# Kernel tuning notes

Hardware: AMD Instinct MI355X
Metric: run time of the kernel (lower is better)

## Reference

```python
import jax, jax.numpy as jnp
import numpy as np

N_NODES = 100000
N_EDGES = 3200000
IN_DIM = 4
HID = 128
OUT_DIM = 4


def setup_inputs() -> dict:
    key = jax.random.key(0)
    ks = jax.random.split(key, 16)
    x = jax.random.normal(ks[0], (N_NODES, IN_DIM), dtype=jnp.float32)
    edge_index = jax.random.randint(ks[1], (2, N_EDGES), 0, N_NODES, dtype=jnp.int32)
    hidden_mask = jax.random.randint(ks[2], (N_NODES,), 0, 2) > 0
    def glorot(k, shape):
        fan_in, fan_out = shape[0], shape[1]
        s = jnp.sqrt(6.0 / (fan_in + fan_out))
        return jax.random.uniform(k, shape, jnp.float32, -s, s)
    return {
        "x": x,
        "edge_index": edge_index,
        "hidden_mask": hidden_mask,
        "W0": glorot(ks[3], (IN_DIM, HID)), "b0": jnp.zeros((HID,), jnp.float32),
        "res_W": glorot(ks[4], (IN_DIM, HID)), "res_b": jnp.zeros((HID,), jnp.float32),
        "W1": glorot(ks[5], (HID, HID)), "b1": jnp.zeros((HID,), jnp.float32),
        "W2": glorot(ks[6], (HID, HID)), "b2": jnp.zeros((HID,), jnp.float32),
        "fc_W": glorot(ks[7], (HID, OUT_DIM)), "fc_b": jnp.zeros((OUT_DIM,), jnp.float32),
    }


def _gcn_norm(edge_index, num_nodes):
    # add self loops, compute symmetric normalization (PyG GCNConv default)
    loop = jnp.arange(num_nodes, dtype=edge_index.dtype)
    src = jnp.concatenate([edge_index[0], loop])
    dst = jnp.concatenate([edge_index[1], loop])
    deg = jax.ops.segment_sum(jnp.ones_like(dst, dtype=jnp.float32), dst,
                              num_segments=num_nodes)
    dis = jnp.where(deg > 0, jax.lax.rsqrt(deg), 0.0)  # deg^{-1/2}, inf -> 0
    norm = dis[src] * dis[dst]  # [E + N]
    return src, dst, norm


def _gcn_conv(h, W, b, src, dst, norm, num_nodes):
    h = h @ W                       # [N, out]
    msg = h[src] * norm[:, None]    # gather + scale, [E+N, out]
    agg = jax.ops.segment_sum(msg, dst, num_segments=num_nodes)
    return agg + b


def reference(x, edge_index, hidden_mask, W0, b0, res_W, res_b, W1, b1, W2, b2, fc_W, fc_b):
    n = x.shape[0]
    src, dst, norm = _gcn_norm(edge_index, n)
    # mask input features (mask broadcast over 4 feature cols)
    h = jnp.where(hidden_mask[:, None], x, 0.0)
    # layer 0: in_dim != hidden -> linear residual
    out0 = _gcn_conv(h, W0, b0, src, dst, norm, n)
    h = jax.nn.relu(out0 + (h @ res_W + res_b))
    # layers 1,2: identity residual
    h = jax.nn.relu(_gcn_conv(h, W1, b1, src, dst, norm, n) + h)
    h = jax.nn.relu(_gcn_conv(h, W2, b2, src, dst, norm, n) + h)
    x_out = h @ fc_W + fc_b
    return (x_out, hidden_mask)
```

## Files before the change

### kernel.cpp

```cpp
#include <hip/hip_runtime.h>
#include <hip/hip_bf16.h>
#include <stdint.h>

#define HID 128
#define NPART 8
#define NCHUNK 256
#define MCHUNK 4096
#define LBITS 10
#define SBITS 22

__global__ void detect_mask_kernel(const unsigned char* __restrict__ p, int nbytes,
                                   int nfloat, int* __restrict__ flags) {
  int stride = blockDim.x * gridDim.x;
  for (int i = blockIdx.x * blockDim.x + threadIdx.x; i < nbytes; i += stride) {
    if ((i & 3) && p[i] != 0) { atomicOr(&flags[0], 1); break; }
  }
  const float* fp = (const float*)p;
  for (int i = blockIdx.x * blockDim.x + threadIdx.x; i < nfloat; i += stride) {
    float f = fp[i];
    if (!(f == 0.0f || f == 1.0f)) { atomicOr(&flags[1], 1); break; }
  }
}

__global__ void expand_mask_h0(const void* __restrict__ maskp, const float4* __restrict__ x4,
                               const int* __restrict__ flags, const float* __restrict__ dis,
                               float* __restrict__ maskout, float* __restrict__ cvec,
                               float4* __restrict__ h0s, int N) {
  int i = blockIdx.x * blockDim.x + threadIdx.x;
  if (i >= N) return;
  float m;
  if (flags[0] == 0)      m = (((const int*)maskp)[i] != 0) ? 1.f : 0.f;
  else if (flags[1] == 0) m = (((const float*)maskp)[i] != 0.f) ? 1.f : 0.f;
  else                    m = (((const unsigned char*)maskp)[i] != 0) ? 1.f : 0.f;
  maskout[i] = m;
  float4 xv = x4[i];
  float4 h0 = make_float4(m * xv.x, m * xv.y, m * xv.z, m * xv.w);
  float* cv = cvec + (size_t)i * 8;
  cv[4] = h0.x; cv[5] = h0.y; cv[6] = h0.z; cv[7] = h0.w;
  float d = dis[i];
  h0s[i] = make_float4(d * h0.x, d * h0.y, d * h0.z, d * h0.w);
}

__global__ void init_gcur_kernel(int* __restrict__ gcur, int n, int CAPB) {
  int i = blockIdx.x * blockDim.x + threadIdx.x;
  if (i < n) gcur[i] = i * CAPB;
}

__global__ void radixA_kernel(const int* __restrict__ src, const int* __restrict__ dst,
                              int* __restrict__ gcur, uint32_t* __restrict__ bdata,
                              int nbin, int CAPB, int E) {
  __shared__ uint32_t sv[MCHUNK];
  __shared__ uint16_t sb[MCHUNK];
  __shared__ int bcnt[1024], boff[1024], gbase[1024];
  __shared__ int wsum[4];
  int t = threadIdx.x;
  int base = blockIdx.x * MCHUNK;
  int m = E - base; if (m > MCHUNK) m = MCHUNK;
  for (int i = t; i < 1024; i += 256) bcnt[i] = 0;
  __syncthreads();
  uint32_t pk[16]; short bn[16];
#pragma unroll
  for (int j = 0; j < 16; j++) {
    int i = base + t + j * 256;
    if (i < base + m) {
      int d = __builtin_nontemporal_load(&dst[i]);
      int s = __builtin_nontemporal_load(&src[i]);
      int b = d >> LBITS;
      pk[j] = ((uint32_t)(d & ((1 << LBITS) - 1)) << SBITS) | (uint32_t)s;
      bn[j] = (short)b;
      atomicAdd(&bcnt[b], 1);
    } else bn[j] = -1;
  }
  __syncthreads();
  {
    int lane = t & 63, w = t >> 6, i0 = t * 4;
    int v0 = bcnt[i0], v1 = bcnt[i0 + 1], v2 = bcnt[i0 + 2], v3 = bcnt[i0 + 3];
    int ts = v0 + v1 + v2 + v3, sc = ts;
    for (int d = 1; d < 64; d <<= 1) { int x = __shfl_up(sc, d, 64); if (lane >= d) sc += x; }
    if (lane == 63) wsum[w] = sc;
    __syncthreads();
    int wo = 0;
    for (int k = 0; k < w; k++) wo += wsum[k];
    int excl = wo + sc - ts;
    boff[i0] = excl; boff[i0 + 1] = excl + v0;
    boff[i0 + 2] = excl + v0 + v1; boff[i0 + 3] = excl + v0 + v1 + v2;
  }
  __syncthreads();
  for (int i = t; i < nbin; i += 256) {
    int c = bcnt[i];
    gbase[i] = c ? atomicAdd(&gcur[i], c) : 0;
  }
  __syncthreads();
  for (int i = t; i < nbin; i += 256) bcnt[i] = boff[i];
  __syncthreads();
#pragma unroll
  for (int j = 0; j < 16; j++) {
    if (bn[j] >= 0) {
      int p = atomicAdd(&bcnt[bn[j]], 1);
      sv[p] = pk[j];
      sb[p] = (uint16_t)bn[j];
    }
  }
  __syncthreads();
  for (int i = t; i < m; i += 256) {
    int b = sb[i];
    int gp = gbase[b] + (i - boff[b]);
    if (gp < (b + 1) * CAPB) bdata[gp] = sv[i];
  }
}

__global__ void bucket_meta_kernel(const int* __restrict__ gcur, int* __restrict__ bstart,
                                   int nbin, int CAPB) {
  __shared__ int wsum[4];
  int t = threadIdx.x, lane = t & 63, w = t >> 6, i0 = t * 4;
  int v[4];
#pragma unroll
  for (int q = 0; q < 4; q++) {
    int i = i0 + q;
    int c = 0;
    if (i < nbin) {
      c = gcur[i] - i * CAPB;
      if (c > CAPB) c = CAPB;
    }
    v[q] = c;
  }
  int ts = v[0] + v[1] + v[2] + v[3], sc = ts;
  for (int d = 1; d < 64; d <<= 1) { int x = __shfl_up(sc, d, 64); if (lane >= d) sc += x; }
  if (lane == 63) wsum[w] = sc;
  __syncthreads();
  int wo = 0;
  for (int k = 0; k < w; k++) wo += wsum[k];
  int excl = wo + sc - ts;
  int e[4] = {excl, excl + v[0], excl + v[0] + v[1], excl + v[0] + v[1] + v[2]};
#pragma unroll
  for (int q = 0; q < 4; q++)
    if (i0 + q < nbin) bstart[i0 + q] = e[q];
  if (t == 255) bstart[nbin] = wo + sc;
}

__global__ void radixB_kernel(const uint32_t* __restrict__ bdata, const int* __restrict__ gcur,
                              const int* __restrict__ bstart, int CAPB,
                              int* __restrict__ off, float* __restrict__ dis,
                              int* __restrict__ csr, int N, int E) {
  __shared__ int cnt[1024], loff[1024];
  __shared__ int wsum[4];
  int b = blockIdx.x, t = threadIdx.x;
  int cb = gcur[b] - b * CAPB; if (cb > CAPB) cb = CAPB;
  int gb = bstart[b];
  const uint32_t* bd = bdata + (size_t)b * CAPB;
  for (int i = t; i < 1024; i += 256) cnt[i] = 0;
  __syncthreads();
  for (int i = t; i < cb; i += 256) atomicAdd(&cnt[bd[i] >> SBITS], 1);
  __syncthreads();
  {
    int lane = t & 63, w = t >> 6, i0 = t * 4;
    int v0 = cnt[i0], v1 = cnt[i0 + 1], v2 = cnt[i0 + 2], v3 = cnt[i0 + 3];
    int ts = v0 + v1 + v2 + v3, sc = ts;
    for (int d = 1; d < 64; d <<= 1) { int x = __shfl_up(sc, d, 64); if (lane >= d) sc += x; }
    if (lane == 63) wsum[w] = sc;
    __syncthreads();
    int wo = 0;
    for (int k = 0; k < w; k++) wo += wsum[k];
    int e0 = wo + sc - ts;
    int e1 = e0 + v0, e2 = e1 + v1, e3 = e2 + v2;
    loff[i0] = e0; loff[i0 + 1] = e1; loff[i0 + 2] = e2; loff[i0 + 3] = e3;
    int d0 = b * 1024 + i0;
    if (d0 + 0 < N) { off[d0 + 0] = gb + e0; dis[d0 + 0] = rsqrtf((float)v0 + 1.0f); }
    if (d0 + 1 < N) { off[d0 + 1] = gb + e1; dis[d0 + 1] = rsqrtf((float)v1 + 1.0f); }
    if (d0 + 2 < N) { off[d0 + 2] = gb + e2; dis[d0 + 2] = rsqrtf((float)v2 + 1.0f); }
    if (d0 + 3 < N) { off[d0 + 3] = gb + e3; dis[d0 + 3] = rsqrtf((float)v3 + 1.0f); }
  }
  if (b == 0 && t == 0) off[N] = E;
  __syncthreads();
  for (int i = t; i < 1024; i += 256) cnt[i] = loff[i];
  __syncthreads();
  for (int i = t; i < cb; i += 256) {
    uint32_t v = bd[i];
    int p = atomicAdd(&cnt[v >> SBITS], 1);
    csr[gb + p] = (int)(v & ((1u << SBITS) - 1));
  }
}

__global__ void scan1_kernel(const int* __restrict__ cnt, int* __restrict__ off,
                             int* __restrict__ bsum, float* __restrict__ dis, int N) {
  __shared__ int wsum[4];
  int t = threadIdx.x, lane = t & 63, w = t >> 6;
  int base = blockIdx.x * 1024 + t * 4;
  int v0 = (base + 0 < N) ? cnt[base + 0] : 0;
  int v1 = (base + 1 < N) ? cnt[base + 1] : 0;
  int v2 = (base + 2 < N) ? cnt[base + 2] : 0;
  int v3 = (base + 3 < N) ? cnt[base + 3] : 0;
  if (dis) {
    if (base + 0 < N) dis[base + 0] = rsqrtf((float)v0 + 1.0f);
    if (base + 1 < N) dis[base + 1] = rsqrtf((float)v1 + 1.0f);
    if (base + 2 < N) dis[base + 2] = rsqrtf((float)v2 + 1.0f);
    if (base + 3 < N) dis[base + 3] = rsqrtf((float)v3 + 1.0f);
  }
  int ts = v0 + v1 + v2 + v3;
  int sc = ts;
  for (int d = 1; d < 64; d <<= 1) {
    int x = __shfl_up(sc, d, 64);
    if (lane >= d) sc += x;
  }
  if (lane == 63) wsum[w] = sc;
  __syncthreads();
  int wo = 0;
  for (int i = 0; i < w; i++) wo += wsum[i];
  int excl = wo + sc - ts;
  if (base + 0 < N) off[base + 0] = excl;
  if (base + 1 < N) off[base + 1] = excl + v0;
  if (base + 2 < N) off[base + 2] = excl + v0 + v1;
  if (base + 3 < N) off[base + 3] = excl + v0 + v1 + v2;
  if (t == 255) bsum[blockIdx.x] = wo + sc;
}

__global__ void scan2_kernel(int* __restrict__ bsum, int nb) {
  if (threadIdx.x == 0 && blockIdx.x == 0) {
    int run = 0;
    for (int i = 0; i < nb; i++) { int v = bsum[i]; bsum[i] = run; run += v; }
  }
}

__global__ void scan3_kernel(int* __restrict__ off, const int* __restrict__ bsum,
                             int* __restrict__ cur, int N, int E) {
  int i = blockIdx.x * blockDim.x + threadIdx.x;
  if (i < N) {
    int o = off[i] + bsum[i >> 10];
    off[i] = o;
    if (cur) cur[i] = o;
  }
  if (i == 0) off[N] = E;
}

__global__ void hist_part_kernel(const int* __restrict__ dst, int* __restrict__ cnt,
                                 int E, int N) {
  int p = blockIdx.x & (NPART - 1);
  int chunk = blockIdx.x >> 3;
  int lo = (int)((long long)p * N / NPART);
  int hi = (int)((long long)(p + 1) * N / NPART);
  int stride = NCHUNK * 256;
  for (int e = chunk * 256 + threadIdx.x; e < E; e += stride) {
    int d = __builtin_nontemporal_load(&dst[e]);
    if (d >= lo && d < hi) atomicAdd(&cnt[d], 1);
  }
}

__global__ void fill_part_kernel(const int* __restrict__ src, const int* __restrict__ dst,
                                 int* __restrict__ cur, int* __restrict__ csr, int E, int N) {
  int p = blockIdx.x & (NPART - 1);
  int chunk = blockIdx.x >> 3;
  int lo = (int)((long long)p * N / NPART);
  int hi = (int)((long long)(p + 1) * N / NPART);
  int stride = NCHUNK * 256;
  for (int e = chunk * 256 + threadIdx.x; e < E; e += stride) {
    int d = __builtin_nontemporal_load(&dst[e]);
    if (d >= lo && d < hi) {
      int s = __builtin_nontemporal_load(&src[e]);
      int pos = atomicAdd(&cur[d], 1);
      csr[pos] = s;
    }
  }
}

__global__ void l0_agg_kernel(const float4* __restrict__ h0s, const float* __restrict__ dis,
                              const int* __restrict__ off, const int* __restrict__ csr,
                              float* __restrict__ cvec, int N) {
  int n = blockIdx.x * blockDim.x + threadIdx.x;
  if (n >= N) return;
  float4 a = h0s[n];
  int e0 = off[n], e1 = off[n + 1];
  int i = e0;
  for (; i < e1 && (i & 3); i++) {
    float4 v = h0s[csr[i]];
    a.x += v.x; a.y += v.y; a.z += v.z; a.w += v.w;
  }
  for (; i + 4 <= e1; i += 4) {
    int4 c = *(const int4*)&csr[i];
    float4 v0 = h0s[c.x], v1 = h0s[c.y], v2 = h0s[c.z], v3 = h0s[c.w];
    a.x += v0.x + v1.x + v2.x + v3.x;
    a.y += v0.y + v1.y + v2.y + v3.y;
    a.z += v0.z + v1.z + v2.z + v3.z;
    a.w += v0.w + v1.w + v2.w + v3.w;
  }
  for (; i < e1; i++) {
    float4 v = h0s[csr[i]];
    a.x += v.x; a.y += v.y; a.z += v.z; a.w += v.w;
  }
  float dn = dis[n];
  float* cv = cvec + (size_t)n * 8;
  cv[0] = dn * a.x; cv[1] = dn * a.y; cv[2] = dn * a.z; cv[3] = dn * a.w;
}

__global__ void l0_combine_kernel(const float* __restrict__ cvec, const float* __restrict__ W0,
                                  const float* __restrict__ b0, const float* __restrict__ resW,
                                  const float* __restrict__ resb, const float* __restrict__ dis,
                                  float* __restrict__ h1, __hip_bfloat16* __restrict__ hbout) {
  int idx = blockIdx.x * blockDim.x + threadIdx.x;
  int n = idx >> 7, c = idx & 127;
  const float* cv = cvec + (size_t)n * 8;
  float acc = b0[c] + resb[c];
#pragma unroll
  for (int k = 0; k < 4; k++) {
    acc += cv[k] * W0[k * HID + c];
    acc += cv[4 + k] * resW[k * HID + c];
  }
  float v = fmaxf(acc, 0.0f);
  h1[idx] = v;
  if (hbout) hbout[idx] = __float2bfloat16(dis[n] * v);
}

#define ACC1(W) { a0 += __uint_as_float((W) << 16); a1 += __uint_as_float((W) & 0xffff0000u); }

__device__ __forceinline__ void gather_tile(const uint32_t* __restrict__ hb,
                                            const float* __restrict__ dis,
                                            const int* __restrict__ off,
                                            const int* __restrict__ csr,
                                            float* __restrict__ ash, int n0, int N) {
  int t = threadIdx.x, lane = t & 63, wv = t >> 6;
  for (int ln = wv * 16; ln < wv * 16 + 16; ln++) {
    int node = n0 + ln;
    float a0 = 0.f, a1 = 0.f;
    if (node < N) {
      uint32_t w = hb[(size_t)node * 64 + lane];
      a0 = __uint_as_float(w << 16);
      a1 = __uint_as_float(w & 0xffff0000u);
      int e0 = off[node], e1 = off[node + 1];
      int i = e0;
      for (; i < e1 && (i & 3); i++) {
        uint32_t ww = hb[(size_t)csr[i] * 64 + lane];
        ACC1(ww)
      }
      for (; i + 16 <= e1; i += 16) {
        int4 c0 = *(const int4*)&csr[i];
        int4 c1 = *(const int4*)&csr[i + 4];
        int4 c2 = *(const int4*)&csr[i + 8];
        int4 c3 = *(const int4*)&csr[i + 12];
        uint32_t w0 = hb[(size_t)c0.x * 64 + lane];
        uint32_t w1 = hb[(size_t)c0.y * 64 + lane];
        uint32_t w2 = hb[(size_t)c0.z * 64 + lane];
        uint32_t w3 = hb[(size_t)c0.w * 64 + lane];
        uint32_t w4 = hb[(size_t)c1.x * 64 + lane];
        uint32_t w5 = hb[(size_t)c1.y * 64 + lane];
        uint32_t w6 = hb[(size_t)c1.z * 64 + lane];
        uint32_t w7 = hb[(size_t)c1.w * 64 + lane];
        uint32_t w8 = hb[(size_t)c2.x * 64 + lane];
        uint32_t w9 = hb[(size_t)c2.y * 64 + lane];
        uint32_t wa = hb[(size_t)c2.z * 64 + lane];
        uint32_t wb = hb[(size_t)c2.w * 64 + lane];
        uint32_t wc = hb[(size_t)c3.x * 64 + lane];
        uint32_t wd = hb[(size_t)c3.y * 64 + lane];
        uint32_t we = hb[(size_t)c3.z * 64 + lane];
        uint32_t wf = hb[(size_t)c3.w * 64 + lane];
        ACC1(w0) ACC1(w1) ACC1(w2) ACC1(w3) ACC1(w4) ACC1(w5) ACC1(w6) ACC1(w7)
        ACC1(w8) ACC1(w9) ACC1(wa) ACC1(wb) ACC1(wc) ACC1(wd) ACC1(we) ACC1(wf)
      }
      for (; i + 4 <= e1; i += 4) {
        int4 c = *(const int4*)&csr[i];
        uint32_t w0 = hb[(size_t)c.x * 64 + lane];
        uint32_t w1 = hb[(size_t)c.y * 64 + lane];
        uint32_t w2 = hb[(size_t)c.z * 64 + lane];
        uint32_t w3 = hb[(size_t)c.w * 64 + lane];
        ACC1(w0) ACC1(w1) ACC1(w2) ACC1(w3)
      }
      for (; i < e1; i++) {
        uint32_t ww = hb[(size_t)csr[i] * 64 + lane];
        ACC1(ww)
      }
      float dn = dis[node];
      a0 *= dn; a1 *= dn;
    }
    *(float2*)&ash[ln * HID + 2 * lane] = make_float2(a0, a1);
  }
}

__global__ void agg_gemm_kernel(const uint32_t* __restrict__ hb, const float* __restrict__ dis,
                                const int* __restrict__ off, const int* __restrict__ csr,
                                const float* __restrict__ hres,
                                const float* __restrict__ W, const float* __restrict__ b,
                                float* __restrict__ hout, __hip_bfloat16* __restrict__ hbout,
                                int N) {
  __shared__ float ash[64 * HID];
  int t = threadIdx.x;
  int n0 = blockIdx.x * 64;
  gather_tile(hb, dis, off, csr, ash, n0, N);
  __syncthreads();
  int tc = t & 31;
  int tn = t >> 5;
  float acc[8][4];
#pragma unroll
  for (int j = 0; j < 8; j++)
#pragma unroll
    for (int q = 0; q < 4; q++) acc[j][q] = 0.0f;

  for (int k = 0; k < HID; k += 4) {
    float4 w0 = *(const float4*)&W[(k + 0) * HID + tc * 4];
    float4 w1 = *(const float4*)&W[(k + 1) * HID + tc * 4];
    float4 w2 = *(const float4*)&W[(k + 2) * HID + tc * 4];
    float4 w3 = *(const float4*)&W[(k + 3) * HID + tc * 4];
#pragma unroll
    for (int j = 0; j < 8; j++) {
      float4 a = *(const float4*)&ash[(tn * 8 + j) * HID + k];
      acc[j][0] += a.x * w0.x + a.y * w1.x + a.z * w2.x + a.w * w3.x;
      acc[j][1] += a.x * w0.y + a.y * w1.y + a.z * w2.y + a.w * w3.y;
      acc[j][2] += a.x * w0.z + a.y * w1.z + a.z * w2.z + a.w * w3.z;
      acc[j][3] += a.x * w0.w + a.y * w1.w + a.z * w2.w + a.w * w3.w;
    }
  }
  float4 bv = *(const float4*)&b[tc * 4];
#pragma unroll
  for (int j = 0; j < 8; j++) {
    int gn = n0 + tn * 8 + j;
    if (gn < N) {
      float4 hv = *(const float4*)&hres[(size_t)gn * HID + tc * 4];
      float4 o;
      o.x = fmaxf(acc[j][0] + bv.x + hv.x, 0.0f);
      o.y = fmaxf(acc[j][1] + bv.y + hv.y, 0.0f);
      o.z = fmaxf(acc[j][2] + bv.z + hv.z, 0.0f);
      o.w = fmaxf(acc[j][3] + bv.w + hv.w, 0.0f);
      *(float4*)&hout[(size_t)gn * HID + tc * 4] = o;
      float dnn = dis[gn];
      __hip_bfloat162 p01 = __float22bfloat162_rn(make_float2(dnn * o.x, dnn * o.y));
      __hip_bfloat162 p23 = __float22bfloat162_rn(make_float2(dnn * o.z, dnn * o.w));
      *(__hip_bfloat162*)&hbout[(size_t)gn * HID + tc * 4] = p01;
      *(__hip_bfloat162*)&hbout[(size_t)gn * HID + tc * 4 + 2] = p23;
    }
  }
}

__global__ void agg_gemm_fc_kernel(const uint32_t* __restrict__ hb, const float* __restrict__ dis,
                                   const int* __restrict__ off, const int* __restrict__ csr,
                                   const float* __restrict__ hres,
                                   const float* __restrict__ W, const float* __restrict__ b,
                                   const float* __restrict__ fcW, const float* __restrict__ fcb,
                                   float* __restrict__ out, int N) {
  __shared__ float ash[64 * HID];
  int t = threadIdx.x;
  int n0 = blockIdx.x * 64;
  gather_tile(hb, dis, off, csr, ash, n0, N);
  __syncthreads();
  int tc = t & 31;
  int tn = t >> 5;
  float acc[8][4];
#pragma unroll
  for (int j = 0; j < 8; j++)
#pragma unroll
    for (int q = 0; q < 4; q++) acc[j][q] = 0.0f;

  for (int k = 0; k < HID; k += 4) {
    float4 w0 = *(const float4*)&W[(k + 0) * HID + tc * 4];
    float4 w1 = *(const float4*)&W[(k + 1) * HID + tc * 4];
    float4 w2 = *(const float4*)&W[(k + 2) * HID + tc * 4];
    float4 w3 = *(const float4*)&W[(k + 3) * HID + tc * 4];
#pragma unroll
    for (int j = 0; j < 8; j++) {
      float4 a = *(const float4*)&ash[(tn * 8 + j) * HID + k];
      acc[j][0] += a.x * w0.x + a.y * w1.x + a.z * w2.x + a.w * w3.x;
      acc[j][1] += a.x * w0.y + a.y * w1.y + a.z * w2.y + a.w * w3.y;
      acc[j][2] += a.x * w0.z + a.y * w1.z + a.z * w2.z + a.w * w3.z;
      acc[j][3] += a.x * w0.w + a.y * w1.w + a.z * w2.w + a.w * w3.w;
    }
  }
  float4 f0 = *(const float4*)&fcW[(tc * 4 + 0) * 4];
  float4 f1 = *(const float4*)&fcW[(tc * 4 + 1) * 4];
  float4 f2 = *(const float4*)&fcW[(tc * 4 + 2) * 4];
  float4 f3 = *(const float4*)&fcW[(tc * 4 + 3) * 4];
  float4 bv = *(const float4*)&b[tc * 4];
  float4 fb = *(const float4*)&fcb[0];
#pragma unroll
  for (int j = 0; j < 8; j++) {
    int gn = n0 + tn * 8 + j;
    float4 o = make_float4(0.f, 0.f, 0.f, 0.f);
    if (gn < N) {
      float4 hv = *(const float4*)&hres[(size_t)gn * HID + tc * 4];
      o.x = fmaxf(acc[j][0] + bv.x + hv.x, 0.0f);
      o.y = fmaxf(acc[j][1] + bv.y + hv.y, 0.0f);
      o.z = fmaxf(acc[j][2] + bv.z + hv.z, 0.0f);
      o.w = fmaxf(acc[j][3] + bv.w + hv.w, 0.0f);
    }
    float r0 = o.x * f0.x + o.y * f1.x + o.z * f2.x + o.w * f3.x;
    float r1 = o.x * f0.y + o.y * f1.y + o.z * f2.y + o.w * f3.y;
    float r2 = o.x * f0.z + o.y * f1.z + o.z * f2.z + o.w * f3.z;
    float r3 = o.x * f0.w + o.y * f1.w + o.z * f2.w + o.w * f3.w;
#pragma unroll
    for (int d = 1; d < 32; d <<= 1) {
      r0 += __shfl_xor(r0, d, 64);
      r1 += __shfl_xor(r1, d, 64);
      r2 += __shfl_xor(r2, d, 64);
      r3 += __shfl_xor(r3, d, 64);
    }
    if (tc == 0 && gn < N)
      *(float4*)&out[(size_t)gn * 4] =
          make_float4(r0 + fb.x, r1 + fb.y, r2 + fb.z, r3 + fb.w);
  }
}

__global__ void agg_hid_kernel(const float* __restrict__ h, const float* __restrict__ dis,
                               const int* __restrict__ off, const int* __restrict__ csr,
                               float* __restrict__ out, int N) {
  int node = blockIdx.x * 4 + (threadIdx.x >> 6);
  int lane = threadIdx.x & 63;
  if (node >= N) return;
  float dn = dis[node];
  const float* hrow = h + (size_t)node * HID;
  float a0 = dn * hrow[lane];
  float a1 = dn * hrow[lane + 64];
  int e0 = off[node], e1 = off[node + 1];
  for (int i = e0; i < e1; i++) {
    int s = csr[i];
    float d = dis[s];
    const float* hs = h + (size_t)s * HID;
    a0 += d * hs[lane];
    a1 += d * hs[lane + 64];
  }
  out[(size_t)node * HID + lane] = dn * a0;
  out[(size_t)node * HID + lane + 64] = dn * a1;
}

__global__ void gemm_resid_relu_kernel(const float* __restrict__ ag, float* __restrict__ hout,
                                       const float* __restrict__ hres,
                                       const float* __restrict__ W, const float* __restrict__ b,
                                       int N) {
  __shared__ float ash[64 * HID];
  int t = threadIdx.x;
  int n0 = blockIdx.x * 64;
  for (int i = t; i < 64 * HID; i += 256) {
    int gn = n0 + (i >> 7);
    ash[i] = (gn < N) ? ag[(size_t)gn * HID + (i & 127)] : 0.0f;
  }
  __syncthreads();
  int tc = t & 31;
  int tn = t >> 5;
  float acc[8][4];
#pragma unroll
  for (int j = 0; j < 8; j++)
#pragma unroll
    for (int q = 0; q < 4; q++) acc[j][q] = 0.0f;
  for (int k = 0; k < HID; k += 4) {
    float4 w0 = *(const float4*)&W[(k + 0) * HID + tc * 4];
    float4 w1 = *(const float4*)&W[(k + 1) * HID + tc * 4];
    float4 w2 = *(const float4*)&W[(k + 2) * HID + tc * 4];
    float4 w3 = *(const float4*)&W[(k + 3) * HID + tc * 4];
#pragma unroll
    for (int j = 0; j < 8; j++) {
      float4 a = *(const float4*)&ash[(tn * 8 + j) * HID + k];
      acc[j][0] += a.x * w0.x + a.y * w1.x + a.z * w2.x + a.w * w3.x;
      acc[j][1] += a.x * w0.y + a.y * w1.y + a.z * w2.y + a.w * w3.y;
      acc[j][2] += a.x * w0.z + a.y * w1.z + a.z * w2.z + a.w * w3.z;
      acc[j][3] += a.x * w0.w + a.y * w1.w + a.z * w2.w + a.w * w3.w;
    }
  }
  float4 bv = *(const float4*)&b[tc * 4];
#pragma unroll
  for (int j = 0; j < 8; j++) {
    int gn = n0 + tn * 8 + j;
    if (gn < N) {
      float4 hv = *(const float4*)&hres[(size_t)gn * HID + tc * 4];
      float4 o;
      o.x = fmaxf(acc[j][0] + bv.x + hv.x, 0.0f);
      o.y = fmaxf(acc[j][1] + bv.y + hv.y, 0.0f);
      o.z = fmaxf(acc[j][2] + bv.z + hv.z, 0.0f);
      o.w = fmaxf(acc[j][3] + bv.w + hv.w, 0.0f);
      *(float4*)&hout[(size_t)gn * HID + tc * 4] = o;
    }
  }
}

__global__ void gemm_resid_fc_kernel(const float* __restrict__ ag,
                                     const float* __restrict__ hres,
                                     const float* __restrict__ W, const float* __restrict__ b,
                                     const float* __restrict__ fcW, const float* __restrict__ fcb,
                                     float* __restrict__ out, int N) {
  __shared__ float ash[64 * HID];
  int t = threadIdx.x;
  int n0 = blockIdx.x * 64;
  for (int i = t; i < 64 * HID; i += 256) {
    int gn = n0 + (i >> 7);
    ash[i] = (gn < N) ? ag[(size_t)gn * HID + (i & 127)] : 0.0f;
  }
  __syncthreads();
  int tc = t & 31;
  int tn = t >> 5;
  float acc[8][4];
#pragma unroll
  for (int j = 0; j < 8; j++)
#pragma unroll
    for (int q = 0; q < 4; q++) acc[j][q] = 0.0f;
  for (int k = 0; k < HID; k += 4) {
    float4 w0 = *(const float4*)&W[(k + 0) * HID + tc * 4];
    float4 w1 = *(const float4*)&W[(k + 1) * HID + tc * 4];
    float4 w2 = *(const float4*)&W[(k + 2) * HID + tc * 4];
    float4 w3 = *(const float4*)&W[(k + 3) * HID + tc * 4];
#pragma unroll
    for (int j = 0; j < 8; j++) {
      float4 a = *(const float4*)&ash[(tn * 8 + j) * HID + k];
      acc[j][0] += a.x * w0.x + a.y * w1.x + a.z * w2.x + a.w * w3.x;
      acc[j][1] += a.x * w0.y + a.y * w1.y + a.z * w2.y + a.w * w3.y;
      acc[j][2] += a.x * w0.z + a.y * w1.z + a.z * w2.z + a.w * w3.z;
      acc[j][3] += a.x * w0.w + a.y * w1.w + a.z * w2.w + a.w * w3.w;
    }
  }
  float4 f0 = *(const float4*)&fcW[(tc * 4 + 0) * 4];
  float4 f1 = *(const float4*)&fcW[(tc * 4 + 1) * 4];
  float4 f2 = *(const float4*)&fcW[(tc * 4 + 2) * 4];
  float4 f3 = *(const float4*)&fcW[(tc * 4 + 3) * 4];
  float4 bv = *(const float4*)&b[tc * 4];
  float4 fb = *(const float4*)&fcb[0];
#pragma unroll
  for (int j = 0; j < 8; j++) {
    int gn = n0 + tn * 8 + j;
    float4 o = make_float4(0.f, 0.f, 0.f, 0.f);
    if (gn < N) {
      float4 hv = *(const float4*)&hres[(size_t)gn * HID + tc * 4];
      o.x = fmaxf(acc[j][0] + bv.x + hv.x, 0.0f);
      o.y = fmaxf(acc[j][1] + bv.y + hv.y, 0.0f);
      o.z = fmaxf(acc[j][2] + bv.z + hv.z, 0.0f);
      o.w = fmaxf(acc[j][3] + bv.w + hv.w, 0.0f);
    }
    float r0 = o.x * f0.x + o.y * f1.x + o.z * f2.x + o.w * f3.x;
    float r1 = o.x * f0.y + o.y * f1.y + o.z * f2.y + o.w * f3.y;
    float r2 = o.x * f0.z + o.y * f1.z + o.z * f2.z + o.w * f3.z;
    float r3 = o.x * f0.w + o.y * f1.w + o.z * f2.w + o.w * f3.w;
#pragma unroll
    for (int d = 1; d < 32; d <<= 1) {
      r0 += __shfl_xor(r0, d, 64);
      r1 += __shfl_xor(r1, d, 64);
      r2 += __shfl_xor(r2, d, 64);
      r3 += __shfl_xor(r3, d, 64);
    }
    if (tc == 0 && gn < N)
      *(float4*)&out[(size_t)gn * 4] =
          make_float4(r0 + fb.x, r1 + fb.y, r2 + fb.z, r3 + fb.w);
  }
}

extern "C" void kernel_launch(void* const* d_in, const int* in_sizes, int n_in,
                              void* d_out, int out_size, void* d_ws, size_t ws_size,
                              hipStream_t stream) {
  const float* x = (const float*)d_in[0];
  const int* edge = (const int*)d_in[1];
  const void* maskp = d_in[2];
  const float* W0 = (const float*)d_in[3];
  const float* b0 = (const float*)d_in[4];
  const float* resW = (const float*)d_in[5];
  const float* resb = (const float*)d_in[6];
  const float* W1 = (const float*)d_in[7];
  const float* b1 = (const float*)d_in[8];
  const float* W2 = (const float*)d_in[9];
  const float* b2 = (const float*)d_in[10];
  const float* fcW = (const float*)d_in[11];
  const float* fcb = (const float*)d_in[12];
  float* out = (float*)d_out;

  int N = in_sizes[0] / 4;
  int E = in_sizes[1] / 2;
  const int* srcp = edge;
  const int* dstp = edge + E;

  char* ws = (char*)d_ws;
  size_t cursor = 0;
  auto alloc = [&](size_t bytes) { char* p = ws + cursor; cursor += (bytes + 511) & ~(size_t)511; return p; };
  int* flags = (int*)alloc(16);
  int* cnt = (int*)alloc((size_t)N * 4);
  float* dis = (float*)alloc((size_t)N * 4);
  int* off = (int*)alloc((size_t)(N + 1) * 4);
  int* bsum = (int*)alloc(1024);
  int nbin = (N + 1023) >> 10;
  int* gcur = (int*)alloc((size_t)(nbin + 1) * 4);
  int* bstart = (int*)alloc((size_t)(nbin + 1) * 4);
  int* csr = (int*)alloc((size_t)E * 4);
  float* h0s = (float*)alloc((size_t)N * 4 * 4);
  float* cvec = (float*)alloc((size_t)N * 8 * 4);
  float* buf0 = (float*)alloc((size_t)N * HID * 4);
  float* buf1 = (float*)alloc((size_t)N * HID * 4);
  size_t base_cursor = cursor;
  __hip_bfloat16* hb1 = (__hip_bfloat16*)alloc((size_t)N * HID * 2);
  __hip_bfloat16* hb2 = (__hip_bfloat16*)alloc((size_t)N * HID * 2);
  bool use_bf16 = (cursor <= ws_size);
  if (!use_bf16) {
    hb1 = nullptr; hb2 = nullptr;
    if (base_cursor > ws_size) return;
  }

  long long expect = (long long)E / (nbin > 0 ? nbin : 1);
  int CAPB = (int)((((expect * 5) / 4 + 127) / 64) * 64);
  if (CAPB < 256) CAPB = 256;
  size_t bdata_bytes = (size_t)nbin * CAPB * 4;
  bool use_radix = (N <= (1 << SBITS)) && (nbin <= 1024) &&
                   (bdata_bytes <= (size_t)N * HID * 4);
  uint32_t* bdata = (uint32_t*)buf1;

  int nThreadsN = (N + 255) / 256;
  int ngemm = (N + 63) / 64;

  hipMemsetAsync(flags, 0, 16, stream);
  detect_mask_kernel<<<256, 256, 0, stream>>>((const unsigned char*)maskp, N, N / 4, flags);

  if (use_radix) {
    init_gcur_kernel<<<(nbin + 255) / 256, 256, 0, stream>>>(gcur, nbin, CAPB);
    radixA_kernel<<<(E + MCHUNK - 1) / MCHUNK, 256, 0, stream>>>(srcp, dstp, gcur, bdata,
                                                                 nbin, CAPB, E);
    bucket_meta_kernel<<<1, 256, 0, stream>>>(gcur, bstart, nbin, CAPB);
    radixB_kernel<<<nbin, 256, 0, stream>>>(bdata, gcur, bstart, CAPB, off, dis, csr, N, E);
  } else {
    hipMemsetAsync(cnt, 0, (size_t)N * 4, stream);
    int nb = (N + 1023) / 1024;
    hist_part_kernel<<<NPART * NCHUNK, 256, 0, stream>>>(dstp, cnt, E, N);
    scan1_kernel<<<nb, 256, 0, stream>>>(cnt, off, bsum, dis, N);
    scan2_kernel<<<1, 64, 0, stream>>>(bsum, nb);
    scan3_kernel<<<nThreadsN, 256, 0, stream>>>(off, bsum, cnt, N, E);
    fill_part_kernel<<<NPART * NCHUNK, 256, 0, stream>>>(srcp, dstp, cnt, csr, E, N);
  }

  expand_mask_h0<<<nThreadsN, 256, 0, stream>>>(maskp, (const float4*)x, flags, dis,
                                                out + (size_t)N * 4, cvec, (float4*)h0s, N);

  l0_agg_kernel<<<nThreadsN, 256, 0, stream>>>((const float4*)h0s, dis, off, csr, cvec, N);
  l0_combine_kernel<<<(N * HID + 255) / 256, 256, 0, stream>>>(cvec, W0, b0, resW, resb, dis,
                                                               buf0, hb1);

  if (use_bf16) {
    agg_gemm_kernel<<<ngemm, 256, 0, stream>>>((const uint32_t*)hb1, dis, off, csr,
                                               buf0, W1, b1, buf1, hb2, N);
    agg_gemm_fc_kernel<<<ngemm, 256, 0, stream>>>((const uint32_t*)hb2, dis, off, csr,
                                                  buf1, W2, b2, fcW, fcb, out, N);
  } else {
    agg_hid_kernel<<<(N + 3) / 4, 256, 0, stream>>>(buf0, dis, off, csr, buf1, N);
    gemm_resid_relu_kernel<<<ngemm, 256, 0, stream>>>(buf1, buf1, buf0, W1, b1, N);
    agg_hid_kernel<<<(N + 3) / 4, 256, 0, stream>>>(buf1, dis, off, csr, buf0, N);
    gemm_resid_fc_kernel<<<ngemm, 256, 0, stream>>>(buf0, buf1, W2, b2, fcW, fcb, out, N);
  }
}
```

Before: 612.6 us.

## Sort CSR neighbors by source chunk and split fused aggregate-GEMM kernels

The radix CSR build now uses 512-node destination bins and sub-sorts each node's neighbor list by coarse source chunk (8 chunks), so gathers walk memory in a more ordered way and hit cache better. The fused gather+GEMM kernels are split into a standalone bf16 aggregation kernel (one wave per node) followed by a GEMM kernel. The fp32 residual copy is dropped: the residual is rebuilt from the dis-scaled bf16 features times a new sqrt(deg) array (rdis). This adds extra kernel launches and an fp32 intermediate round trip, and the residual loses precision to bf16.

```diff
diff --git a/kernel.cpp b/kernel.cpp
--- a/kernel.cpp
+++ b/kernel.cpp
@@ -6,8 +6,9 @@
 #define NPART 8
 #define NCHUNK 256
 #define MCHUNK 4096
-#define LBITS 10
+#define LBITS 9
 #define SBITS 22
+#define NCH 8
 
 __global__ void detect_mask_kernel(const unsigned char* __restrict__ p, int nbytes,
                                    int nfloat, int* __restrict__ flags) {
@@ -141,43 +142,65 @@
 __global__ void radixB_kernel(const uint32_t* __restrict__ bdata, const int* __restrict__ gcur,
                               const int* __restrict__ bstart, int CAPB,
                               int* __restrict__ off, float* __restrict__ dis,
-                              int* __restrict__ csr, int N, int E) {
-  __shared__ int cnt[1024], loff[1024];
+                              float* __restrict__ rdis, int* __restrict__ csr,
+                              int N, int E, int cshift) {
+  __shared__ int cnt[4096], loff[4096];
   __shared__ int wsum[4];
   int b = blockIdx.x, t = threadIdx.x;
   int cb = gcur[b] - b * CAPB; if (cb > CAPB) cb = CAPB;
   int gb = bstart[b];
   const uint32_t* bd = bdata + (size_t)b * CAPB;
-  for (int i = t; i < 1024; i += 256) cnt[i] = 0;
-  __syncthreads();
-  for (int i = t; i < cb; i += 256) atomicAdd(&cnt[bd[i] >> SBITS], 1);
-  __syncthreads();
-  {
-    int lane = t & 63, w = t >> 6, i0 = t * 4;
-    int v0 = cnt[i0], v1 = cnt[i0 + 1], v2 = cnt[i0 + 2], v3 = cnt[i0 + 3];
-    int ts = v0 + v1 + v2 + v3, sc = ts;
-    for (int d = 1; d < 64; d <<= 1) { int x = __shfl_up(sc, d, 64); if (lane >= d) sc += x; }
-    if (lane == 63) wsum[w] = sc;
-    __syncthreads();
-    int wo = 0;
-    for (int k = 0; k < w; k++) wo += wsum[k];
-    int e0 = wo + sc - ts;
-    int e1 = e0 + v0, e2 = e1 + v1, e3 = e2 + v2;
-    loff[i0] = e0; loff[i0 + 1] = e1; loff[i0 + 2] = e2; loff[i0 + 3] = e3;
-    int d0 = b * 1024 + i0;
-    if (d0 + 0 < N) { off[d0 + 0] = gb + e0; dis[d0 + 0] = rsqrtf((float)v0 + 1.0f); }
-    if (d0 + 1 < N) { off[d0 + 1] = gb + e1; dis[d0 + 1] = rsqrtf((float)v1 + 1.0f); }
-    if (d0 + 2 < N) { off[d0 + 2] = gb + e2; dis[d0 + 2] = rsqrtf((float)v2 + 1.0f); }
-    if (d0 + 3 < N) { off[d0 + 3] = gb + e3; dis[d0 + 3] = rsqrtf((float)v3 + 1.0f); }
-  }
-  if (b == 0 && t == 0) off[N] = E;
-  __syncthreads();
-  for (int i = t; i < 1024; i += 256) cnt[i] = loff[i];
-  __syncthreads();
+  for (int i = t; i < 4096; i += 256) cnt[i] = 0;
+  __syncthreads();
+  const uint32_t smask = (1u << SBITS) - 1;
   for (int i = t; i < cb; i += 256) {
     uint32_t v = bd[i];
-    int p = atomicAdd(&cnt[v >> SBITS], 1);
-    csr[gb + p] = (int)(v & ((1u << SBITS) - 1));
+    int ld = v >> SBITS;
+    int src = (int)(v & smask);
+    atomicAdd(&cnt[(ld << 3) | (src >> cshift)], 1);
+  }
+  __syncthreads();
+  int lane = t & 63, w = t >> 6;
+  int loc[16];
+  int s = 0;
+  int base16 = t * 16;
+#pragma unroll
+  for (int q = 0; q < 16; q++) { loc[q] = cnt[base16 + q]; s += loc[q]; }
+  int sc = s;
+  for (int d = 1; d < 64; d <<= 1) { int x = __shfl_up(sc, d, 64); if (lane >= d) sc += x; }
+  if (lane == 63) wsum[w] = sc;
+  __syncthreads();
+  int wo = 0;
+  for (int k = 0; k < w; k++) wo += wsum[k];
+  int excl = wo + sc - s;
+  {
+    int run = excl;
+#pragma unroll
+    for (int q = 0; q < 16; q++) { loff[base16 + q] = run; run += loc[q]; }
+  }
+  int c0 = loc[0] + loc[1] + loc[2] + loc[3] + loc[4] + loc[5] + loc[6] + loc[7];
+  int c1 = loc[8] + loc[9] + loc[10] + loc[11] + loc[12] + loc[13] + loc[14] + loc[15];
+  int dst0 = b * (1 << LBITS) + 2 * t;
+  if (dst0 < N) {
+    off[dst0] = gb + excl;
+    dis[dst0] = rsqrtf((float)c0 + 1.0f);
+    rdis[dst0] = sqrtf((float)c0 + 1.0f);
+  }
+  if (dst0 + 1 < N) {
+    off[dst0 + 1] = gb + excl + c0;
+    dis[dst0 + 1] = rsqrtf((float)c1 + 1.0f);
+    rdis[dst0 + 1] = sqrtf((float)c1 + 1.0f);
+  }
+  if (b == 0 && t == 0) off[N] = E;
+  __syncthreads();
+  for (int i = t; i < 4096; i += 256) cnt[i] = loff[i];
+  __syncthreads();
+  for (int i = t; i < cb; i += 256) {
+    uint32_t v = bd[i];
+    int ld = v >> SBITS;
+    int src = (int)(v & smask);
+    int p = atomicAdd(&cnt[(ld << 3) | (src >> cshift)], 1);
+    csr[gb + p] = src;
   }
 }
 
@@ -305,193 +328,53 @@
     acc += cv[4 + k] * resW[k * HID + c];
   }
   float v = fmaxf(acc, 0.0f);
-  h1[idx] = v;
+  if (h1) h1[idx] = v;
   if (hbout) hbout[idx] = __float2bfloat16(dis[n] * v);
 }
 
 #define ACC1(W) { a0 += __uint_as_float((W) << 16); a1 += __uint_as_float((W) & 0xffff0000u); }
-
-__device__ __forceinline__ void gather_tile(const uint32_t* __restrict__ hb,
-                                            const float* __restrict__ dis,
-                                            const int* __restrict__ off,
-                                            const int* __restrict__ csr,
-                                            float* __restrict__ ash, int n0, int N) {
-  int t = threadIdx.x, lane = t & 63, wv = t >> 6;
-  for (int ln = wv * 16; ln < wv * 16 + 16; ln++) {
-    int node = n0 + ln;
-    float a0 = 0.f, a1 = 0.f;
-    if (node < N) {
-      uint32_t w = hb[(size_t)node * 64 + lane];
-      a0 = __uint_as_float(w << 16);
-      a1 = __uint_as_float(w & 0xffff0000u);
-      int e0 = off[node], e1 = off[node + 1];
-      int i = e0;
-      for (; i < e1 && (i & 3); i++) {
-        uint32_t ww = hb[(size_t)csr[i] * 64 + lane];
-        ACC1(ww)
-      }
-      for (; i + 16 <= e1; i += 16) {
-        int4 c0 = *(const int4*)&csr[i];
-        int4 c1 = *(const int4*)&csr[i + 4];
-        int4 c2 = *(const int4*)&csr[i + 8];
-        int4 c3 = *(const int4*)&csr[i + 12];
-        uint32_t w0 = hb[(size_t)c0.x * 64 + lane];
-        uint32_t w1 = hb[(size_t)c0.y * 64 + lane];
-        uint32_t w2 = hb[(size_t)c0.z * 64 + lane];
-        uint32_t w3 = hb[(size_t)c0.w * 64 + lane];
-        uint32_t w4 = hb[(size_t)c1.x * 64 + lane];
-        uint32_t w5 = hb[(size_t)c1.y * 64 + lane];
-        uint32_t w6 = hb[(size_t)c1.z * 64 + lane];
-        uint32_t w7 = hb[(size_t)c1.w * 64 + lane];
-        uint32_t w8 = hb[(size_t)c2.x * 64 + lane];
-        uint32_t w9 = hb[(size_t)c2.y * 64 + lane];
-        uint32_t wa = hb[(size_t)c2.z * 64 + lane];
-        uint32_t wb = hb[(size_t)c2.w * 64 + lane];
-        uint32_t wc = hb[(size_t)c3.x * 64 + lane];
-        uint32_t wd = hb[(size_t)c3.y * 64 + lane];
-        uint32_t we = hb[(size_t)c3.z * 64 + lane];
-        uint32_t wf = hb[(size_t)c3.w * 64 + lane];
-        ACC1(w0) ACC1(w1) ACC1(w2) ACC1(w3) ACC1(w4) ACC1(w5) ACC1(w6) ACC1(w7)
-        ACC1(w8) ACC1(w9) ACC1(wa) ACC1(wb) ACC1(wc) ACC1(wd) ACC1(we) ACC1(wf)
-      }
-      for (; i + 4 <= e1; i += 4) {
-        int4 c = *(const int4*)&csr[i];
-        uint32_t w0 = hb[(size_t)c.x * 64 + lane];
-        uint32_t w1 = hb[(size_t)c.y * 64 + lane];
-        uint32_t w2 = hb[(size_t)c.z * 64 + lane];
-        uint32_t w3 = hb[(size_t)c.w * 64 + lane];
-        ACC1(w0) ACC1(w1) ACC1(w2) ACC1(w3)
-      }
-      for (; i < e1; i++) {
-        uint32_t ww = hb[(size_t)csr[i] * 64 + lane];
-        ACC1(ww)
-      }
-      float dn = dis[node];
-      a0 *= dn; a1 *= dn;
-    }
-    *(float2*)&ash[ln * HID + 2 * lane] = make_float2(a0, a1);
-  }
-}
-
-__global__ void agg_gemm_kernel(const uint32_t* __restrict__ hb, const float* __restrict__ dis,
-                                const int* __restrict__ off, const int* __restrict__ csr,
-                                const float* __restrict__ hres,
-                                const float* __restrict__ W, const float* __restrict__ b,
-                                float* __restrict__ hout, __hip_bfloat16* __restrict__ hbout,
-                                int N) {
-  __shared__ float ash[64 * HID];
-  int t = threadIdx.x;
-  int n0 = blockIdx.x * 64;
-  gather_tile(hb, dis, off, csr, ash, n0, N);
-  __syncthreads();
-  int tc = t & 31;
-  int tn = t >> 5;
-  float acc[8][4];
-#pragma unroll
-  for (int j = 0; j < 8; j++)
-#pragma unroll
-    for (int q = 0; q < 4; q++) acc[j][q] = 0.0f;
-
-  for (int k = 0; k < HID; k += 4) {
-    float4 w0 = *(const float4*)&W[(k + 0) * HID + tc * 4];
-    float4 w1 = *(const float4*)&W[(k + 1) * HID + tc * 4];
-    float4 w2 = *(const float4*)&W[(k + 2) * HID + tc * 4];
-    float4 w3 = *(const float4*)&W[(k + 3) * HID + tc * 4];
-#pragma unroll
-    for (int j = 0; j < 8; j++) {
-      float4 a = *(const float4*)&ash[(tn * 8 + j) * HID + k];
-      acc[j][0] += a.x * w0.x + a.y * w1.x + a.z * w2.x + a.w * w3.x;
-      acc[j][1] += a.x * w0.y + a.y * w1.y + a.z * w2.y + a.w * w3.y;
-      acc[j][2] += a.x * w0.z + a.y * w1.z + a.z * w2.z + a.w * w3.z;
-      acc[j][3] += a.x * w0.w + a.y * w1.w + a.z * w2.w + a.w * w3.w;
-    }
-  }
-  float4 bv = *(const float4*)&b[tc * 4];
-#pragma unroll
-  for (int j = 0; j < 8; j++) {
-    int gn = n0 + tn * 8 + j;
-    if (gn < N) {
-      float4 hv = *(const float4*)&hres[(size_t)gn * HID + tc * 4];
-      float4 o;
-      o.x = fmaxf(acc[j][0] + bv.x + hv.x, 0.0f);
-      o.y = fmaxf(acc[j][1] + bv.y + hv.y, 0.0f);
-      o.z = fmaxf(acc[j][2] + bv.z + hv.z, 0.0f);
-      o.w = fmaxf(acc[j][3] + bv.w + hv.w, 0.0f);
-      *(float4*)&hout[(size_t)gn * HID + tc * 4] = o;
-      float dnn = dis[gn];
-      __hip_bfloat162 p01 = __float22bfloat162_rn(make_float2(dnn * o.x, dnn * o.y));
-      __hip_bfloat162 p23 = __float22bfloat162_rn(make_float2(dnn * o.z, dnn * o.w));
-      *(__hip_bfloat162*)&hbout[(size_t)gn * HID + tc * 4] = p01;
-      *(__hip_bfloat162*)&hbout[(size_t)gn * HID + tc * 4 + 2] = p23;
-    }
-  }
-}
-
-__global__ void agg_gemm_fc_kernel(const uint32_t* __restrict__ hb, const float* __restrict__ dis,
-                                   const int* __restrict__ off, const int* __restrict__ csr,
-                                   const float* __restrict__ hres,
-                                   const float* __restrict__ W, const float* __restrict__ b,
-                                   const float* __restrict__ fcW, const float* __restrict__ fcb,
-                                   float* __restrict__ out, int N) {
-  __shared__ float ash[64 * HID];
-  int t = threadIdx.x;
-  int n0 = blockIdx.x * 64;
-  gather_tile(hb, dis, off, csr, ash, n0, N);
-  __syncthreads();
-  int tc = t & 31;
-  int tn = t >> 5;
-  float acc[8][4];
-#pragma unroll
-  for (int j = 0; j < 8; j++)
-#pragma unroll
-    for (int q = 0; q < 4; q++) acc[j][q] = 0.0f;
-
-  for (int k = 0; k < HID; k += 4) {
-    float4 w0 = *(const float4*)&W[(k + 0) * HID + tc * 4];
-    float4 w1 = *(const float4*)&W[(k + 1) * HID + tc * 4];
-    float4 w2 = *(const float4*)&W[(k + 2) * HID + tc * 4];
-    float4 w3 = *(const float4*)&W[(k + 3) * HID + tc * 4];
-#pragma unroll
-    for (int j = 0; j < 8; j++) {
-      float4 a = *(const float4*)&ash[(tn * 8 + j) * HID + k];
-      acc[j][0] += a.x * w0.x + a.y * w1.x + a.z * w2.x + a.w * w3.x;
-      acc[j][1] += a.x * w0.y + a.y * w1.y + a.z * w2.y + a.w * w3.y;
-      acc[j][2] += a.x * w0.z + a.y * w1.z + a.z * w2.z + a.w * w3.z;
-      acc[j][3] += a.x * w0.w + a.y * w1.w + a.z * w2.w + a.w * w3.w;
-    }
-  }
-  float4 f0 = *(const float4*)&fcW[(tc * 4 + 0) * 4];
-  float4 f1 = *(const float4*)&fcW[(tc * 4 + 1) * 4];
-  float4 f2 = *(const float4*)&fcW[(tc * 4 + 2) * 4];
-  float4 f3 = *(const float4*)&fcW[(tc * 4 + 3) * 4];
-  float4 bv = *(const float4*)&b[tc * 4];
-  float4 fb = *(const float4*)&fcb[0];
-#pragma unroll
-  for (int j = 0; j < 8; j++) {
-    int gn = n0 + tn * 8 + j;
-    float4 o = make_float4(0.f, 0.f, 0.f, 0.f);
-    if (gn < N) {
-      float4 hv = *(const float4*)&hres[(size_t)gn * HID + tc * 4];
-      o.x = fmaxf(acc[j][0] + bv.x + hv.x, 0.0f);
-      o.y = fmaxf(acc[j][1] + bv.y + hv.y, 0.0f);
-      o.z = fmaxf(acc[j][2] + bv.z + hv.z, 0.0f);
-      o.w = fmaxf(acc[j][3] + bv.w + hv.w, 0.0f);
-    }
-    float r0 = o.x * f0.x + o.y * f1.x + o.z * f2.x + o.w * f3.x;
-    float r1 = o.x * f0.y + o.y * f1.y + o.z * f2.y + o.w * f3.y;
-    float r2 = o.x * f0.z + o.y * f1.z + o.z * f2.z + o.w * f3.z;
-    float r3 = o.x * f0.w + o.y * f1.w + o.z * f2.w + o.w * f3.w;
-#pragma unroll
-    for (int d = 1; d < 32; d <<= 1) {
-      r0 += __shfl_xor(r0, d, 64);
-      r1 += __shfl_xor(r1, d, 64);
-      r2 += __shfl_xor(r2, d, 64);
-      r3 += __shfl_xor(r3, d, 64);
-    }
-    if (tc == 0 && gn < N)
-      *(float4*)&out[(size_t)gn * 4] =
-          make_float4(r0 + fb.x, r1 + fb.y, r2 + fb.z, r3 + fb.w);
-  }
+__global__ void agg_hid_bf16_kernel(const uint32_t* __restrict__ hb, const float* __restrict__ dis,
+                                    const int* __restrict__ off, const int* __restrict__ csr,
+                                    float* __restrict__ out, int N) {
+  int node = blockIdx.x * 4 + (threadIdx.x >> 6);
+  int lane = threadIdx.x & 63;
+  if (node >= N) return;
+  uint32_t w = hb[(size_t)node * 64 + lane];
+  float a0 = __uint_as_float(w << 16);
+  float a1 = __uint_as_float(w & 0xffff0000u);
+  int e0 = off[node], e1 = off[node + 1];
+  int i = e0;
+  for (; i < e1 && (i & 3); i++) {
+    uint32_t ww = hb[(size_t)csr[i] * 64 + lane];
+    ACC1(ww)
+  }
+  for (; i + 8 <= e1; i += 8) {
+    int4 c0 = *(const int4*)&csr[i];
+    int4 c1 = *(const int4*)&csr[i + 4];
+    uint32_t w0 = hb[(size_t)c0.x * 64 + lane];
+    uint32_t w1 = hb[(size_t)c0.y * 64 + lane];
+    uint32_t w2 = hb[(size_t)c0.z * 64 + lane];
+    uint32_t w3 = hb[(size_t)c0.w * 64 + lane];
+    uint32_t w4 = hb[(size_t)c1.x * 64 + lane];
+    uint32_t w5 = hb[(size_t)c1.y * 64 + lane];
+    uint32_t w6 = hb[(size_t)c1.z * 64 + lane];
+    uint32_t w7 = hb[(size_t)c1.w * 64 + lane];
+    ACC1(w0) ACC1(w1) ACC1(w2) ACC1(w3) ACC1(w4) ACC1(w5) ACC1(w6) ACC1(w7)
+  }
+  for (; i + 4 <= e1; i += 4) {
+    int4 c = *(const int4*)&csr[i];
+    uint32_t w0 = hb[(size_t)c.x * 64 + lane];
+    uint32_t w1 = hb[(size_t)c.y * 64 + lane];
+    uint32_t w2 = hb[(size_t)c.z * 64 + lane];
+    uint32_t w3 = hb[(size_t)c.w * 64 + lane];
+    ACC1(w0) ACC1(w1) ACC1(w2) ACC1(w3)
+  }
+  for (; i < e1; i++) {
+    uint32_t ww = hb[(size_t)csr[i] * 64 + lane];
+    ACC1(ww)
+  }
+  float dn = dis[node];
+  *(float2*)&out[(size_t)node * HID + 2 * lane] = make_float2(dn * a0, dn * a1);
 }
 
 __global__ void agg_hid_kernel(const float* __restrict__ h, const float* __restrict__ dis,
@@ -516,10 +399,142 @@
   out[(size_t)node * HID + lane + 64] = dn * a1;
 }
 
-__global__ void gemm_resid_relu_kernel(const float* __restrict__ ag, float* __restrict__ hout,
-                                       const float* __restrict__ hres,
+__global__ void gemm_resid_relu_kernel(const float* __restrict__ ag,
+                                       const __hip_bfloat16* __restrict__ hbres,
+                                       const float* __restrict__ rdis,
                                        const float* __restrict__ W, const float* __restrict__ b,
-                                       int N) {
+                                       const float* __restrict__ dis,
+                                       __hip_bfloat16* __restrict__ hbout, int N) {
+  __shared__ float ash[64 * HID];
+  int t = threadIdx.x;
+  int n0 = blockIdx.x * 64;
+  for (int i = t; i < 64 * HID; i += 256) {
+    int gn = n0 + (i >> 7);
+    ash[i] = (gn < N) ? ag[(size_t)gn * HID + (i & 127)] : 0.0f;
+  }
+  __syncthreads();
+  int tc = t & 31;
+  int tn = t >> 5;
+  float acc[8][4];
+#pragma unroll
+  for (int j = 0; j < 8; j++)
+#pragma unroll
+    for (int q = 0; q < 4; q++) acc[j][q] = 0.0f;
+
+  for (int k = 0; k < HID; k += 4) {
+    float4 w0 = *(const float4*)&W[(k + 0) * HID + tc * 4];
+    float4 w1 = *(const float4*)&W[(k + 1) * HID + tc * 4];
+    float4 w2 = *(const float4*)&W[(k + 2) * HID + tc * 4];
+    float4 w3 = *(const float4*)&W[(k + 3) * HID + tc * 4];
+#pragma unroll
+    for (int j = 0; j < 8; j++) {
+      float4 a = *(const float4*)&ash[(tn * 8 + j) * HID + k];
+      acc[j][0] += a.x * w0.x + a.y * w1.x + a.z * w2.x + a.w * w3.x;
+      acc[j][1] += a.x * w0.y + a.y * w1.y + a.z * w2.y + a.w * w3.y;
+      acc[j][2] += a.x * w0.z + a.y * w1.z + a.z * w2.z + a.w * w3.z;
+      acc[j][3] += a.x * w0.w + a.y * w1.w + a.z * w2.w + a.w * w3.w;
+    }
+  }
+  float4 bv = *(const float4*)&b[tc * 4];
+#pragma unroll
+  for (int j = 0; j < 8; j++) {
+    int gn = n0 + tn * 8 + j;
+    if (gn < N) {
+      float rd = rdis[gn];
+      uint2 hu = *(const uint2*)&hbres[(size_t)gn * HID + tc * 4];
+      float h0v = __uint_as_float(hu.x << 16) * rd;
+      float h1v = __uint_as_float(hu.x & 0xffff0000u) * rd;
+      float h2v = __uint_as_float(hu.y << 16) * rd;
+      float h3v = __uint_as_float(hu.y & 0xffff0000u) * rd;
+      float4 o;
+      o.x = fmaxf(acc[j][0] + bv.x + h0v, 0.0f);
+      o.y = fmaxf(acc[j][1] + bv.y + h1v, 0.0f);
+      o.z = fmaxf(acc[j][2] + bv.z + h2v, 0.0f);
+      o.w = fmaxf(acc[j][3] + bv.w + h3v, 0.0f);
+      float dnn = dis[gn];
+      __hip_bfloat162 p01 = __float22bfloat162_rn(make_float2(dnn * o.x, dnn * o.y));
+      __hip_bfloat162 p23 = __float22bfloat162_rn(make_float2(dnn * o.z, dnn * o.w));
+      *(__hip_bfloat162*)&hbout[(size_t)gn * HID + tc * 4] = p01;
+      *(__hip_bfloat162*)&hbout[(size_t)gn * HID + tc * 4 + 2] = p23;
+    }
+  }
+}
+
+__global__ void gemm_resid_fc_kernel(const float* __restrict__ ag,
+                                     const __hip_bfloat16* __restrict__ hbres,
+                                     const float* __restrict__ rdis,
+                                     const float* __restrict__ W, const float* __restrict__ b,
+                                     const float* __restrict__ fcW, const float* __restrict__ fcb,
+                                     float* __restrict__ out, int N) {
+  __shared__ float ash[64 * HID];
+  int t = threadIdx.x;
+  int n0 = blockIdx.x * 64;
+  for (int i = t; i < 64 * HID; i += 256) {
+    int gn = n0 + (i >> 7);
+    ash[i] = (gn < N) ? ag[(size_t)gn * HID + (i & 127)] : 0.0f;
+  }
+  __syncthreads();
+  int tc = t & 31;
+  int tn = t >> 5;
+  float acc[8][4];
+#pragma unroll
+  for (int j = 0; j < 8; j++)
+#pragma unroll
+    for (int q = 0; q < 4; q++) acc[j][q] = 0.0f;
+
+  for (int k = 0; k < HID; k += 4) {
+    float4 w0 = *(const float4*)&W[(k + 0) * HID + tc * 4];
+    float4 w1 = *(const float4*)&W[(k + 1) * HID + tc * 4];
+    float4 w2 = *(const float4*)&W[(k + 2) * HID + tc * 4];
+    float4 w3 = *(const float4*)&W[(k + 3) * HID + tc * 4];
+#pragma unroll
+    for (int j = 0; j < 8; j++) {
+      float4 a = *(const float4*)&ash[(tn * 8 + j) * HID + k];
+      acc[j][0] += a.x * w0.x + a.y * w1.x + a.z * w2.x + a.w * w3.x;
+      acc[j][1] += a.x * w0.y + a.y * w1.y + a.z * w2.y + a.w * w3.y;
+      acc[j][2] += a.x * w0.z + a.y * w1.z + a.z * w2.z + a.w * w3.z;
+      acc[j][3] += a.x * w0.w + a.y * w1.w + a.z * w2.w + a.w * w3.w;
+    }
+  }
+  float4 f0 = *(const float4*)&fcW[(tc * 4 + 0) * 4];
+  float4 f1 = *(const float4*)&fcW[(tc * 4 + 1) * 4];
+  float4 f2 = *(const float4*)&fcW[(tc * 4 + 2) * 4];
+  float4 f3 = *(const float4*)&fcW[(tc * 4 + 3) * 4];
+  float4 bv = *(const float4*)&b[tc * 4];
+  float4 fb = *(const float4*)&fcb[0];
+#pragma unroll
+  for (int j = 0; j < 8; j++) {
+    int gn = n0 + tn * 8 + j;
+    float4 o = make_float4(0.f, 0.f, 0.f, 0.f);
+    if (gn < N) {
+      float rd = rdis[gn];
+      uint2 hu = *(const uint2*)&hbres[(size_t)gn * HID + tc * 4];
+      o.x = fmaxf(acc[j][0] + bv.x + __uint_as_float(hu.x << 16) * rd, 0.0f);
+      o.y = fmaxf(acc[j][1] + bv.y + __uint_as_float(hu.x & 0xffff0000u) * rd, 0.0f);
+      o.z = fmaxf(acc[j][2] + bv.z + __uint_as_float(hu.y << 16) * rd, 0.0f);
+      o.w = fmaxf(acc[j][3] + bv.w + __uint_as_float(hu.y & 0xffff0000u) * rd, 0.0f);
+    }
+    float r0 = o.x * f0.x + o.y * f1.x + o.z * f2.x + o.w * f3.x;
+    float r1 = o.x * f0.y + o.y * f1.y + o.z * f2.y + o.w * f3.y;
+    float r2 = o.x * f0.z + o.y * f1.z + o.z * f2.z + o.w * f3.z;
+    float r3 = o.x * f0.w + o.y * f1.w + o.z * f2.w + o.w * f3.w;
+#pragma unroll
+    for (int d = 1; d < 32; d <<= 1) {
+      r0 += __shfl_xor(r0, d, 64);
+      r1 += __shfl_xor(r1, d, 64);
+      r2 += __shfl_xor(r2, d, 64);
+      r3 += __shfl_xor(r3, d, 64);
+    }
+    if (tc == 0 && gn < N)
+      *(float4*)&out[(size_t)gn * 4] =
+          make_float4(r0 + fb.x, r1 + fb.y, r2 + fb.z, r3 + fb.w);
+  }
+}
+
+__global__ void gemm_resid_relu_f32_kernel(const float* __restrict__ ag, float* __restrict__ hout,
+                                           const float* __restrict__ hres,
+                                           const float* __restrict__ W, const float* __restrict__ b,
+                                           int N) {
   __shared__ float ash[64 * HID];
   int t = threadIdx.x;
   int n0 = blockIdx.x * 64;
@@ -565,11 +580,11 @@
   }
 }
 
-__global__ void gemm_resid_fc_kernel(const float* __restrict__ ag,
-                                     const float* __restrict__ hres,
-                                     const float* __restrict__ W, const float* __restrict__ b,
-                                     const float* __restrict__ fcW, const float* __restrict__ fcb,
-                                     float* __restrict__ out, int N) {
+__global__ void gemm_resid_fc_f32_kernel(const float* __restrict__ ag,
+                                         const float* __restrict__ hres,
+                                         const float* __restrict__ W, const float* __restrict__ b,
+                                         const float* __restrict__ fcW, const float* __restrict__ fcb,
+                                         float* __restrict__ out, int N) {
   __shared__ float ash[64 * HID];
   int t = threadIdx.x;
   int n0 = blockIdx.x * 64;
@@ -662,9 +677,10 @@
   int* flags = (int*)alloc(16);
   int* cnt = (int*)alloc((size_t)N * 4);
   float* dis = (float*)alloc((size_t)N * 4);
+  float* rdis = (float*)alloc((size_t)N * 4);
   int* off = (int*)alloc((size_t)(N + 1) * 4);
   int* bsum = (int*)alloc(1024);
-  int nbin = (N + 1023) >> 10;
+  int nbin = (N + (1 << LBITS) - 1) >> LBITS;
   int* gcur = (int*)alloc((size_t)(nbin + 1) * 4);
   int* bstart = (int*)alloc((size_t)(nbin + 1) * 4);
   int* csr = (int*)alloc((size_t)E * 4);
@@ -689,6 +705,9 @@
                    (bdata_bytes <= (size_t)N * HID * 4);
   uint32_t* bdata = (uint32_t*)buf1;
 
+  int cshift = 0;
+  while (((N - 1) >> cshift) > (NCH - 1)) cshift++;
+
   int nThreadsN = (N + 255) / 256;
   int ngemm = (N + 63) / 64;
 
@@ -700,7 +719,8 @@
     radixA_kernel<<<(E + MCHUNK - 1) / MCHUNK, 256, 0, stream>>>(srcp, dstp, gcur, bdata,
                                                                  nbin, CAPB, E);
     bucket_meta_kernel<<<1, 256, 0, stream>>>(gcur, bstart, nbin, CAPB);
-    radixB_kernel<<<nbin, 256, 0, stream>>>(bdata, gcur, bstart, CAPB, off, dis, csr, N, E);
+    radixB_kernel<<<nbin, 256, 0, stream>>>(bdata, gcur, bstart, CAPB, off, dis, rdis,
+                                            csr, N, E, cshift);
   } else {
     hipMemsetAsync(cnt, 0, (size_t)N * 4, stream);
     int nb = (N + 1023) / 1024;
@@ -715,18 +735,22 @@
                                                 out + (size_t)N * 4, cvec, (float4*)h0s, N);
 
   l0_agg_kernel<<<nThreadsN, 256, 0, stream>>>((const float4*)h0s, dis, off, csr, cvec, N);
-  l0_combine_kernel<<<(N * HID + 255) / 256, 256, 0, stream>>>(cvec, W0, b0, resW, resb, dis,
-                                                               buf0, hb1);
 
   if (use_bf16) {
-    agg_gemm_kernel<<<ngemm, 256, 0, stream>>>((const uint32_t*)hb1, dis, off, csr,
-                                               buf0, W1, b1, buf1, hb2, N);
-    agg_gemm_fc_kernel<<<ngemm, 256, 0, stream>>>((const uint32_t*)hb2, dis, off, csr,
-                                                  buf1, W2, b2, fcW, fcb, out, N);
+    l0_combine_kernel<<<(N * HID + 255) / 256, 256, 0, stream>>>(cvec, W0, b0, resW, resb, dis,
+                                                                 nullptr, hb1);
+    agg_hid_bf16_kernel<<<(N + 3) / 4, 256, 0, stream>>>((const uint32_t*)hb1, dis, off, csr,
+                                                         buf0, N);
+    gemm_resid_relu_kernel<<<ngemm, 256, 0, stream>>>(buf0, hb1, rdis, W1, b1, dis, hb2, N);
+    agg_hid_bf16_kernel<<<(N + 3) / 4, 256, 0, stream>>>((const uint32_t*)hb2, dis, off, csr,
+                                                         buf0, N);
+    gemm_resid_fc_kernel<<<ngemm, 256, 0, stream>>>(buf0, hb2, rdis, W2, b2, fcW, fcb, out, N);
   } else {
+    l0_combine_kernel<<<(N * HID + 255) / 256, 256, 0, stream>>>(cvec, W0, b0, resW, resb, dis,
+                                                                 buf0, nullptr);
     agg_hid_kernel<<<(N + 3) / 4, 256, 0, stream>>>(buf0, dis, off, csr, buf1, N);
-    gemm_resid_relu_kernel<<<ngemm, 256, 0, stream>>>(buf1, buf1, buf0, W1, b1, N);
+    gemm_resid_relu_f32_kernel<<<ngemm, 256, 0, stream>>>(buf1, buf1, buf0, W1, b1, N);
     agg_hid_kernel<<<(N + 3) / 4, 256, 0, stream>>>(buf1, dis, off, csr, buf0, N);
-    gemm_resid_fc_kernel<<<ngemm, 256, 0, stream>>>(buf0, buf1, W2, b2, fcW, fcb, out, N);
-  }
-}
+    gemm_resid_fc_f32_kernel<<<ngemm, 256, 0, stream>>>(buf0, buf1, W2, b2, fcW, fcb, out, N);
+  }
+}
```

After: 521.7 us. -14.8%, faster.
